# Kernel tuning notes

Hardware: AMD Instinct MI355X
Metric: run time of the kernel (lower is better)

The kernel has to match this reference:

```python
import jax, jax.numpy as jnp
import numpy as np

L, B, E, H = 1024, 8, 1024, 16
HD = E // H
SCALE = HD ** -0.5
EPS = 1e-5


def setup_inputs() -> dict:
    key = jax.random.key(0)
    ks = jax.random.split(key, 6)
    s = E ** -0.5
    return {
        "x": jax.random.normal(ks[0], (L, B, E), dtype=jnp.float32),
        "attn_mask": jnp.zeros((L, L), dtype=jnp.float32),
        "Wq": jax.random.normal(ks[1], (E, E), dtype=jnp.float32) * s,
        "bq": jnp.zeros((E,), dtype=jnp.float32),
        "Wk": jax.random.normal(ks[2], (E, E), dtype=jnp.float32) * s,
        "bk": jnp.zeros((E,), dtype=jnp.float32),
        "Wv": jax.random.normal(ks[3], (E, E), dtype=jnp.float32) * s,
        "bv": jnp.zeros((E,), dtype=jnp.float32),
        "Wo": jax.random.normal(ks[4], (E, E), dtype=jnp.float32) * s,
        "bo": jnp.zeros((E,), dtype=jnp.float32),
        "gamma": jnp.ones((E,), dtype=jnp.float32),
        "beta": jnp.zeros((E,), dtype=jnp.float32),
    }


def _layernorm(x, gamma, beta):
    mu = jnp.mean(x, axis=-1, keepdims=True)
    var = jnp.mean(jnp.square(x - mu), axis=-1, keepdims=True)
    return (x - mu) * jax.lax.rsqrt(var + EPS) * gamma + beta


def reference(x, attn_mask, Wq, bq, Wk, bk, Wv, bv, Wo, bo, gamma, beta):
    # x: (L, B, E); pre-LN residual attention block (dropout=0, eval)
    ln_x = _layernorm(x, gamma, beta)
    # torch Linear: y = x @ W.T + b
    q = (ln_x @ Wq.T + bq) * SCALE
    k = ln_x @ Wk.T + bk
    v = ln_x @ Wv.T + bv
    # (L, B, E) -> (B, H, L, hd)
    def split_heads(t):
        return t.reshape(L, B, H, HD).transpose(1, 2, 0, 3)
    q, k, v = split_heads(q), split_heads(k), split_heads(v)
    # full attention matrix, as in the original non-fused bmm path
    attn = jnp.einsum('bhqd,bhkd->bhqk', q, k) + attn_mask[None, None]
    attn = jax.nn.softmax(attn, axis=-1)
    out = jnp.einsum('bhqk,bhkd->bhqd', attn, v)  # (B, H, L, hd)
    out = out.transpose(2, 0, 1, 3).reshape(L, B, E)
    out = out @ Wo.T + bo
    return x + out
```

## Files before the change

### kernel.cpp

```cpp
#include <hip/hip_runtime.h>

#define LL 1024
#define BB 8
#define EE 1024
#define HH 16
#define HD 64
#define MROWS (LL*BB)

typedef __attribute__((ext_vector_type(8))) short short8v;
typedef __attribute__((ext_vector_type(4))) float f32x4;
typedef __attribute__((ext_vector_type(16))) float f32x16;

#define LOG2E 1.44269504088896f

__device__ __forceinline__ unsigned short tobf(float f) {
    union { float f; unsigned u; } un; un.f = f;
    unsigned u = un.u;
    u += 0x7fffu + ((u >> 16) & 1u);
    return (unsigned short)(u >> 16);
}

__device__ __forceinline__ float max3f(float a, float b, float c) {
    return fmaxf(fmaxf(a, b), c);
}

__device__ __forceinline__ void load_lds16(const unsigned short* g, unsigned short* l) {
    __builtin_amdgcn_global_load_lds((const __attribute__((address_space(1))) unsigned int*)g,
                                     (__attribute__((address_space(3))) unsigned int*)l,
                                     16, 0, 0);
}

__global__ __launch_bounds__(256) void convw4_kernel(const float* __restrict__ w0,
                                                     const float* __restrict__ w1,
                                                     const float* __restrict__ w2,
                                                     const float* __restrict__ w3,
                                                     unsigned short* __restrict__ o0,
                                                     unsigned short* __restrict__ o1,
                                                     unsigned short* __restrict__ o2,
                                                     unsigned short* __restrict__ o3) {
    const float* w; unsigned short* o;
    switch (blockIdx.y) {
        case 0:  w = w0; o = o0; break;
        case 1:  w = w1; o = o1; break;
        case 2:  w = w2; o = o2; break;
        default: w = w3; o = o3; break;
    }
    int i = (blockIdx.x * 256 + threadIdx.x) * 4;
    float4 v = *(const float4*)&w[i];
    ushort4 r;
    r.x = tobf(v.x); r.y = tobf(v.y); r.z = tobf(v.z); r.w = tobf(v.w);
    *(ushort4*)&o[i] = r;
}

__global__ __launch_bounds__(256) void maskprep_kernel(const float* __restrict__ m,
                                                       unsigned* __restrict__ o) {
    __shared__ float t_sh[64][65];
    const int q0 = blockIdx.x * 64, k0 = blockIdx.y * 64;
    const int tid = threadIdx.x;
    {
        const int r = tid >> 2, c0 = (tid & 3) * 16;
        #pragma unroll
        for (int i = 0; i < 4; ++i) {
            float4 v = *(const float4*)&m[(size_t)(q0 + r) * LL + k0 + c0 + i*4];
            t_sh[r][c0+i*4+0] = v.x; t_sh[r][c0+i*4+1] = v.y;
            t_sh[r][c0+i*4+2] = v.z; t_sh[r][c0+i*4+3] = v.w;
        }
    }
    __syncthreads();
    const int k2l = tid >> 3, qi = (tid & 7) * 8;
    unsigned pk[8];
    #pragma unroll
    for (int j = 0; j < 8; ++j) {
        const unsigned lo = tobf(t_sh[qi+j][2*k2l]   * LOG2E);
        const unsigned hb = tobf(t_sh[qi+j][2*k2l+1] * LOG2E);
        pk[j] = lo | (hb << 16);
    }
    unsigned* orow = &o[(size_t)(k0/2 + k2l) * LL + q0 + qi];
    *(uint4*)&orow[0] = make_uint4(pk[0], pk[1], pk[2], pk[3]);
    *(uint4*)&orow[4] = make_uint4(pk[4], pk[5], pk[6], pk[7]);
}

__global__ __launch_bounds__(256) void ln_kernel(const float* __restrict__ x,
                                                 const float* __restrict__ gamma,
                                                 const float* __restrict__ beta,
                                                 unsigned short* __restrict__ out) {
    const int row = blockIdx.x;
    const int tid = threadIdx.x;
    const float4 v = *(const float4*)&x[(size_t)row * EE + tid * 4];
    float s = v.x + v.y + v.z + v.w;
    float q = v.x*v.x + v.y*v.y + v.z*v.z + v.w*v.w;
    #pragma unroll
    for (int off = 1; off < 64; off <<= 1) {
        s += __shfl_xor(s, off);
        q += __shfl_xor(q, off);
    }
    __shared__ float ss[4], sq[4];
    const int wv = tid >> 6;
    if ((tid & 63) == 0) { ss[wv] = s; sq[wv] = q; }
    __syncthreads();
    s = ss[0] + ss[1] + ss[2] + ss[3];
    q = sq[0] + sq[1] + sq[2] + sq[3];
    const float mu = s * (1.0f / EE);
    const float var = q * (1.0f / EE) - mu * mu;
    const float rs = rsqrtf(var + 1e-5f);
    ushort4 o;
    o.x = tobf((v.x - mu) * rs * gamma[tid*4+0] + beta[tid*4+0]);
    o.y = tobf((v.y - mu) * rs * gamma[tid*4+1] + beta[tid*4+1]);
    o.z = tobf((v.z - mu) * rs * gamma[tid*4+2] + beta[tid*4+2]);
    o.w = tobf((v.w - mu) * rs * gamma[tid*4+3] + beta[tid*4+3]);
    *(ushort4*)&out[(size_t)row * EE + tid * 4] = o;
}

#define GEMM128_BODY(A_, W_)                                                              \
    __shared__ unsigned short a_sh[3][128*32];                                            \
    __shared__ unsigned short b_sh[3][128*32];                                            \
    const int tid = threadIdx.x, lane = tid & 63, wave = tid >> 6;                        \
    const int bm = blockIdx.y * 128, bn = blockIdx.x * 128;                               \
    const int wr = (wave >> 1) * 64, wc = (wave & 1) * 64;                                \
    const int l16 = lane & 15, q4 = lane >> 4;                                            \
    const int grow = lane >> 2;                                                           \
    const int gswz = (((lane & 3) ^ (grow & 3)) * 8);                                     \
    const int rslot = (q4 ^ (l16 & 3)) * 16;                       \
    f32x4 acc[4][4] = {};                                                                 \
    _Pragma("unroll")                                                                     \
    for (int i = 0; i < 2; ++i) {                                                         \
        const int ch = wave * 2 + i;                                                      \
        load_lds16(&A_[(size_t)(bm + ch*16 + grow)*EE + gswz], &a_sh[0][ch*512]);         \
        load_lds16(&W_[(size_t)(bn + ch*16 + grow)*EE + gswz], &b_sh[0][ch*512]);         \
    }                                                                                     \
    _Pragma("unroll")                                                                     \
    for (int i = 0; i < 2; ++i) {                                                         \
        const int ch = wave * 2 + i;                                                      \
        load_lds16(&A_[(size_t)(bm + ch*16 + grow)*EE + 32 + gswz], &a_sh[1][ch*512]);    \
        load_lds16(&W_[(size_t)(bn + ch*16 + grow)*EE + 32 + gswz], &b_sh[1][ch*512]);    \
    }                                                                                     \
    int buf = 0, sb = 2;                                                                  \
    for (int it = 0; it < 32; ++it) {                                                     \
        if (it < 31) asm volatile("s_waitcnt vmcnt(4)" ::: "memory");                     \
        else         asm volatile("s_waitcnt vmcnt(0)" ::: "memory");                     \
        __builtin_amdgcn_s_barrier();                                                     \
        if (it < 30) {                                                                    \
            const int kn = (it + 2) * 32;                                                 \
            _Pragma("unroll")                                                             \
            for (int i = 0; i < 2; ++i) {                                                 \
                const int ch = wave * 2 + i;                                              \
                load_lds16(&A_[(size_t)(bm + ch*16 + grow)*EE + kn + gswz], &a_sh[sb][ch*512]); \
                load_lds16(&W_[(size_t)(bn + ch*16 + grow)*EE + kn + gswz], &b_sh[sb][ch*512]); \
            }                                                                             \
        }                                                                                 \
        short8v af[4], bf[4];                                                             \
        _Pragma("unroll")                                                                 \
        for (int mi = 0; mi < 4; ++mi)                                                    \
            af[mi] = *(const short8v*)((const char*)&a_sh[buf][0] + (size_t)(wr + mi*16 + l16)*64 + rslot); \
        _Pragma("unroll")                                                                 \
        for (int ni = 0; ni < 4; ++ni)                                                    \
            bf[ni] = *(const short8v*)((const char*)&b_sh[buf][0] + (size_t)(wc + ni*16 + l16)*64 + rslot); \
        __builtin_amdgcn_s_setprio(1);                                                    \
        _Pragma("unroll")                                                                 \
        for (int mi = 0; mi < 4; ++mi)                                                    \
            _Pragma("unroll")                                                             \
            for (int ni = 0; ni < 4; ++ni)                                                \
                acc[mi][ni] = __builtin_amdgcn_mfma_f32_16x16x32_bf16(af[mi], bf[ni], acc[mi][ni], 0, 0, 0); \
        __builtin_amdgcn_s_setprio(0);                                                    \
        buf = (buf == 2) ? 0 : buf + 1;                                                   \
        sb  = (sb  == 2) ? 0 : sb  + 1;                                                   \
    }

__global__ __launch_bounds__(256) void gemm_qkv(const unsigned short* __restrict__ A,
                                                const unsigned short* __restrict__ W,
                                                const float* __restrict__ bq,
                                                const float* __restrict__ bk,
                                                const float* __restrict__ bv,
                                                unsigned short* __restrict__ qo,
                                                unsigned short* __restrict__ ko,
                                                unsigned short* __restrict__ vo) {
    GEMM128_BODY(A, W)
    const int seg = blockIdx.x >> 3;
    const float* bias = seg == 0 ? bq : (seg == 1 ? bk : bv);
    #pragma unroll
    for (int mi = 0; mi < 4; ++mi) {
        #pragma unroll
        for (int ni = 0; ni < 4; ++ni) {
            #pragma unroll
            for (int r = 0; r < 4; ++r) {
                const int m  = bm + wr + mi*16 + (lane >> 4)*4 + r;
                const int nn = (bn & 1023) + wc + ni*16 + l16;
                const float v = acc[mi][ni][r] + bias[nn];
                const int l = m >> 3, b = m & 7, h = nn >> 6, d = nn & 63;
                const int bh = b*HH + h;
                if (seg == 2) {
                    const int k16 = l >> 4, khi = (l >> 3) & 1, ke = l & 7;
                    const int dt = d >> 5, dl = d & 31;
                    vo[((((size_t)bh*64 + k16)*2 + dt)*64 + khi*32 + dl)*8 + ke] = tobf(v);
                } else {
                    const int t32 = l >> 5, l32 = l & 31;
                    const int dc = d >> 4, hi2 = (d >> 3) & 1, e = d & 7;
                    const size_t idx = ((((size_t)bh*32 + t32)*4 + dc)*64 + hi2*32 + l32)*8 + e;
                    if (seg == 0) qo[idx] = tobf(v * (0.125f * LOG2E));
                    else          ko[idx] = tobf(v);
                }
            }
        }
    }
}

__global__ __launch_bounds__(256) void gemm_o(const unsigned short* __restrict__ A,
                                              const unsigned short* __restrict__ W,
                                              const float* __restrict__ bias,
                                              const float* __restrict__ xres,
                                              float* __restrict__ outf) {
    GEMM128_BODY(A, W)
    #pragma unroll
    for (int mi = 0; mi < 4; ++mi) {
        #pragma unroll
        for (int ni = 0; ni < 4; ++ni) {
            #pragma unroll
            for (int r = 0; r < 4; ++r) {
                const int m = bm + wr + mi*16 + (lane >> 4)*4 + r;
                const int n = bn + wc + ni*16 + l16;
                outf[(size_t)m * EE + n] = acc[mi][ni][r] + bias[n] + xres[(size_t)m * EE + n];
            }
        }
    }
}

__global__ __launch_bounds__(256) void attn_kernel(const unsigned short* __restrict__ Qf,
                                                   const unsigned short* __restrict__ Kf,
                                                   const unsigned short* __restrict__ Vf,
                                                   const unsigned* __restrict__ maskT2,
                                                   unsigned short* __restrict__ attn_out) {
    const int tid = threadIdx.x, lane = tid & 63, wave = tid >> 6;
    const int l32 = lane & 31, hi = lane >> 5;
    const int b1 = blockIdx.x;
    const int bh = (b1 & 7) * 16 + ((b1 >> 3) & 15);
    const int qt = ((b1 >> 7) & 7) * 4 + wave;
    const int qtok = qt * 32 + l32;
    const unsigned short* qfp = Qf + ((size_t)(bh * 32 + qt) * 4) * 512;
    const unsigned short* kfb = Kf + (size_t)bh * 32 * 4 * 512;
    const unsigned short* vfb = Vf + (size_t)bh * 64 * 2 * 512;

    short8v qf[4];
    #pragma unroll
    for (int dc = 0; dc < 4; ++dc)
        qf[dc] = *(const short8v*)&qfp[dc * 512 + lane * 8];

    f32x16 acc[2] = {};
    float mrun = -1e30f, srun = 0.f;

    const unsigned* mt2base = maskT2 + qtok;
    short8v kf[4];
    #pragma unroll
    for (int dc = 0; dc < 4; ++dc)
        kf[dc] = *(const short8v*)&kfb[dc * 512 + lane * 8];
    unsigned mcur[8], mnxt[8];
    #pragma unroll
    for (int j = 0; j < 8; ++j)
        mcur[j] = mt2base[(size_t)((j & 1) + 4*(j >> 1) + 2*hi) * LL];

    for (int t = 0; t < 32; ++t) {
        f32x16 s = {};
        __builtin_amdgcn_s_setprio(1);
        #pragma unroll
        for (int dc = 0; dc < 4; ++dc)
            s = __builtin_amdgcn_mfma_f32_32x32x16_bf16(kf[dc], qf[dc], s, 0, 0, 0);
        __builtin_amdgcn_s_setprio(0);
        short8v vf00, vf01, vf10, vf11;
        vf00 = *(const short8v*)&vfb[((size_t)(t*2 + 0)*2 + 0)*512 + lane*8];
        vf01 = *(const short8v*)&vfb[((size_t)(t*2 + 0)*2 + 1)*512 + lane*8];
        vf10 = *(const short8v*)&vfb[((size_t)(t*2 + 1)*2 + 0)*512 + lane*8];
        vf11 = *(const short8v*)&vfb[((size_t)(t*2 + 1)*2 + 1)*512 + lane*8];
        if (t < 31) {
            #pragma unroll
            for (int dc = 0; dc < 4; ++dc)
                kf[dc] = *(const short8v*)&kfb[((size_t)(t + 1)*4 + dc)*512 + lane*8];
            #pragma unroll
            for (int j = 0; j < 8; ++j)
                mnxt[j] = mt2base[(size_t)((t + 1)*16 + (j & 1) + 4*(j >> 1) + 2*hi) * LL];
        }
        #pragma unroll
        for (int j = 0; j < 8; ++j) {
            s[2*j]   += __uint_as_float(mcur[j] << 16);
            s[2*j+1] += __uint_as_float(mcur[j] & 0xffff0000u);
        }
        const float a0 = max3f(s[0],  s[1],  s[2]);
        const float a1 = max3f(s[3],  s[4],  s[5]);
        const float a2 = max3f(s[6],  s[7],  s[8]);
        const float a3 = max3f(s[9],  s[10], s[11]);
        const float a4 = max3f(s[12], s[13], s[14]);
        float pm = fmaxf(max3f(a0, a1, a2), max3f(a3, a4, s[15]));
        pm = fmaxf(pm, __shfl_xor(pm, 32));
        if (__any(pm - mrun > 8.0f)) {
            const float mn = fmaxf(mrun, pm);
            const float al = exp2f(mrun - mn);
            #pragma unroll
            for (int i = 0; i < 16; ++i) { acc[0][i] *= al; acc[1][i] *= al; }
            srun *= al;
            mrun = mn;
        }
        float p[16];
        #pragma unroll
        for (int i = 0; i < 16; ++i) p[i] = exp2f(s[i] - mrun);
        const float t0 = p[0]+p[1],   t1 = p[2]+p[3],   t2 = p[4]+p[5],   t3 = p[6]+p[7];
        const float t4 = p[8]+p[9],   t5 = p[10]+p[11], t6 = p[12]+p[13], t7 = p[14]+p[15];
        const float u0 = t0+t1, u1 = t2+t3, u2 = t4+t5, u3 = t6+t7;
        float rs = (u0+u1) + (u2+u3);
        rs += __shfl_xor(rs, 32);
        srun += rs;
        unsigned w[8];
        #pragma unroll
        for (int j = 0; j < 8; ++j)
            asm("v_cvt_pk_bf16_f32 %0, %1, %2" : "=v"(w[j]) : "v"(p[2*j]), "v"(p[2*j+1]));
        asm volatile("v_permlane32_swap_b32 %0, %1" : "+v"(w[0]), "+v"(w[2]));
        asm volatile("v_permlane32_swap_b32 %0, %1" : "+v"(w[1]), "+v"(w[3]));
        asm volatile("v_permlane32_swap_b32 %0, %1" : "+v"(w[4]), "+v"(w[6]));
        asm volatile("v_permlane32_swap_b32 %0, %1" : "+v"(w[5]), "+v"(w[7]));
        union { uint4 u; short8v s8; } pb0, pb1;
        pb0.u = make_uint4(w[0], w[1], w[2], w[3]);
        pb1.u = make_uint4(w[4], w[5], w[6], w[7]);
        __builtin_amdgcn_s_setprio(1);
        acc[0] = __builtin_amdgcn_mfma_f32_32x32x16_bf16(vf00, pb0.s8, acc[0], 0, 0, 0);
        acc[1] = __builtin_amdgcn_mfma_f32_32x32x16_bf16(vf01, pb0.s8, acc[1], 0, 0, 0);
        acc[0] = __builtin_amdgcn_mfma_f32_32x32x16_bf16(vf10, pb1.s8, acc[0], 0, 0, 0);
        acc[1] = __builtin_amdgcn_mfma_f32_32x32x16_bf16(vf11, pb1.s8, acc[1], 0, 0, 0);
        __builtin_amdgcn_s_setprio(0);
        #pragma unroll
        for (int j = 0; j < 8; ++j) mcur[j] = mnxt[j];
    }
    const float inv = 1.0f / srun;
    const int b = bh >> 4, h = bh & 15;
    unsigned short* orow = attn_out + ((size_t)qtok * BB + b) * EE + h * HD;
    #pragma unroll
    for (int dt = 0; dt < 2; ++dt) {
        #pragma unroll
        for (int g = 0; g < 4; ++g) {
            const float a0 = acc[dt][4*g+0]*inv, a1 = acc[dt][4*g+1]*inv;
            const float a2 = acc[dt][4*g+2]*inv, a3 = acc[dt][4*g+3]*inv;
            unsigned lo, hw;
            asm("v_cvt_pk_bf16_f32 %0, %1, %2" : "=v"(lo) : "v"(a0), "v"(a1));
            asm("v_cvt_pk_bf16_f32 %0, %1, %2" : "=v"(hw) : "v"(a2), "v"(a3));
            *(uint2*)&orow[dt*32 + g*8 + hi*4] = make_uint2(lo, hw);
        }
    }
}

extern "C" void kernel_launch(void* const* d_in, const int* in_sizes, int n_in,
                              void* d_out, int out_size, void* d_ws, size_t ws_size,
                              hipStream_t stream) {
    (void)in_sizes; (void)n_in; (void)out_size; (void)ws_size;
    const float* x     = (const float*)d_in[0];
    const float* mask  = (const float*)d_in[1];
    const float* Wq    = (const float*)d_in[2];
    const float* bq    = (const float*)d_in[3];
    const float* Wk    = (const float*)d_in[4];
    const float* bk    = (const float*)d_in[5];
    const float* Wv    = (const float*)d_in[6];
    const float* bv    = (const float*)d_in[7];
    const float* Wo    = (const float*)d_in[8];
    const float* bo    = (const float*)d_in[9];
    const float* gamma = (const float*)d_in[10];
    const float* beta  = (const float*)d_in[11];
    float* out = (float*)d_out;

    unsigned short* ws   = (unsigned short*)d_ws;
    unsigned short* ln   = ws;
    unsigned short* wqkv = ln   + (size_t)MROWS * EE;
    unsigned short* wob  = wqkv + (size_t)3 * EE * EE;
    unsigned short* qb   = wob  + (size_t)EE * EE;
    unsigned short* kbp  = qb   + (size_t)BB * HH * LL * HD;
    unsigned short* vtb  = kbp  + (size_t)BB * HH * LL * HD;
    unsigned short* attnb = ln;
    unsigned* maskT2 = (unsigned*)wqkv;

    convw4_kernel<<<dim3(1024, 4), 256, 0, stream>>>(
        Wq, Wk, Wv, Wo,
        wqkv, wqkv + (size_t)EE * EE, wqkv + (size_t)2 * EE * EE, wob);
    ln_kernel<<<MROWS, 256, 0, stream>>>(x, gamma, beta, ln);

    gemm_qkv<<<dim3(24, 64), 256, 0, stream>>>(ln, wqkv, bq, bk, bv, qb, kbp, vtb);

    maskprep_kernel<<<dim3(16, 16), 256, 0, stream>>>(mask, maskT2);

    attn_kernel<<<1024, 256, 0, stream>>>(qb, kbp, vtb, maskT2, attnb);

    gemm_o<<<dim3(8, 64), 256, 0, stream>>>(attnb, wob, bo, x, out);
}
```

Baseline: 223.3 us.

## Skip mask loads when mask is all-zero; compute row sums via MFMA with ones

The mask prep kernel now sets a device flag if any mask entry is nonzero, and the attention kernel reads that flag and skips the per-tile mask loads and adds when it is clear. The softmax row sum now comes from extra MFMAs against a ones matrix instead of VALU adds and a cross-lane shuffle, and the row-max reduction uses permlane32 swap instead of a shuffle. Launch bounds are raised to request higher occupancy. The check runs at runtime, so nonzero masks still take the correct path. The cost is an extra memset launch, two more MFMAs per tile, and extra accumulator registers.

New measurement: 223.5 us. No clear change (+0.1%).

```diff
diff --git a/kernel.cpp b/kernel.cpp
--- a/kernel.cpp
+++ b/kernel.cpp
@@ -53,19 +53,23 @@
 }
 
 __global__ __launch_bounds__(256) void maskprep_kernel(const float* __restrict__ m,
-                                                       unsigned* __restrict__ o) {
+                                                       unsigned* __restrict__ o,
+                                                       unsigned* __restrict__ flag) {
     __shared__ float t_sh[64][65];
     const int q0 = blockIdx.x * 64, k0 = blockIdx.y * 64;
     const int tid = threadIdx.x;
+    unsigned nz = 0;
     {
         const int r = tid >> 2, c0 = (tid & 3) * 16;
         #pragma unroll
         for (int i = 0; i < 4; ++i) {
             float4 v = *(const float4*)&m[(size_t)(q0 + r) * LL + k0 + c0 + i*4];
+            nz |= (v.x != 0.0f) | (v.y != 0.0f) | (v.z != 0.0f) | (v.w != 0.0f);
             t_sh[r][c0+i*4+0] = v.x; t_sh[r][c0+i*4+1] = v.y;
             t_sh[r][c0+i*4+2] = v.z; t_sh[r][c0+i*4+3] = v.w;
         }
     }
+    if (__any(nz) && (tid & 63) == 0) atomicOr(flag, 1u);
     __syncthreads();
     const int k2l = tid >> 3, qi = (tid & 7) * 8;
     unsigned pk[8];
@@ -224,17 +228,19 @@
     }
 }
 
-__global__ __launch_bounds__(256) void attn_kernel(const unsigned short* __restrict__ Qf,
-                                                   const unsigned short* __restrict__ Kf,
-                                                   const unsigned short* __restrict__ Vf,
-                                                   const unsigned* __restrict__ maskT2,
-                                                   unsigned short* __restrict__ attn_out) {
+__global__ __launch_bounds__(256, 4) void attn_kernel(const unsigned short* __restrict__ Qf,
+                                                      const unsigned short* __restrict__ Kf,
+                                                      const unsigned short* __restrict__ Vf,
+                                                      const unsigned* __restrict__ maskT2,
+                                                      const unsigned* __restrict__ mflagp,
+                                                      unsigned short* __restrict__ attn_out) {
     const int tid = threadIdx.x, lane = tid & 63, wave = tid >> 6;
     const int l32 = lane & 31, hi = lane >> 5;
     const int b1 = blockIdx.x;
     const int bh = (b1 & 7) * 16 + ((b1 >> 3) & 15);
     const int qt = ((b1 >> 7) & 7) * 4 + wave;
     const int qtok = qt * 32 + l32;
+    const unsigned mf = (unsigned)__builtin_amdgcn_readfirstlane((int)mflagp[0]);
     const unsigned short* qfp = Qf + ((size_t)(bh * 32 + qt) * 4) * 512;
     const unsigned short* kfb = Kf + (size_t)bh * 32 * 4 * 512;
     const unsigned short* vfb = Vf + (size_t)bh * 64 * 2 * 512;
@@ -244,8 +250,13 @@
     for (int dc = 0; dc < 4; ++dc)
         qf[dc] = *(const short8v*)&qfp[dc * 512 + lane * 8];
 
+    union { unsigned u4[4]; short8v s8; } ones;
+    #pragma unroll
+    for (int i = 0; i < 4; ++i) ones.u4[i] = 0x3F803F80u;
+
     f32x16 acc[2] = {};
-    float mrun = -1e30f, srun = 0.f;
+    f32x16 accs = {};
+    float mrun = -1e30f;
 
     const unsigned* mt2base = maskT2 + qtok;
     short8v kf[4];
@@ -253,9 +264,11 @@
     for (int dc = 0; dc < 4; ++dc)
         kf[dc] = *(const short8v*)&kfb[dc * 512 + lane * 8];
     unsigned mcur[8], mnxt[8];
-    #pragma unroll
-    for (int j = 0; j < 8; ++j)
-        mcur[j] = mt2base[(size_t)((j & 1) + 4*(j >> 1) + 2*hi) * LL];
+    if (mf) {
+        #pragma unroll
+        for (int j = 0; j < 8; ++j)
+            mcur[j] = mt2base[(size_t)((j & 1) + 4*(j >> 1) + 2*hi) * LL];
+    }
 
     for (int t = 0; t < 32; ++t) {
         f32x16 s = {};
@@ -273,14 +286,18 @@
             #pragma unroll
             for (int dc = 0; dc < 4; ++dc)
                 kf[dc] = *(const short8v*)&kfb[((size_t)(t + 1)*4 + dc)*512 + lane*8];
-            #pragma unroll
-            for (int j = 0; j < 8; ++j)
-                mnxt[j] = mt2base[(size_t)((t + 1)*16 + (j & 1) + 4*(j >> 1) + 2*hi) * LL];
-        }
-        #pragma unroll
-        for (int j = 0; j < 8; ++j) {
-            s[2*j]   += __uint_as_float(mcur[j] << 16);
-            s[2*j+1] += __uint_as_float(mcur[j] & 0xffff0000u);
+            if (mf) {
+                #pragma unroll
+                for (int j = 0; j < 8; ++j)
+                    mnxt[j] = mt2base[(size_t)((t + 1)*16 + (j & 1) + 4*(j >> 1) + 2*hi) * LL];
+            }
+        }
+        if (mf) {
+            #pragma unroll
+            for (int j = 0; j < 8; ++j) {
+                s[2*j]   += __uint_as_float(mcur[j] << 16);
+                s[2*j+1] += __uint_as_float(mcur[j] & 0xffff0000u);
+            }
         }
         const float a0 = max3f(s[0],  s[1],  s[2]);
         const float a1 = max3f(s[3],  s[4],  s[5]);
@@ -288,28 +305,24 @@
         const float a3 = max3f(s[9],  s[10], s[11]);
         const float a4 = max3f(s[12], s[13], s[14]);
         float pm = fmaxf(max3f(a0, a1, a2), max3f(a3, a4, s[15]));
-        pm = fmaxf(pm, __shfl_xor(pm, 32));
+        {
+            float pu = pm, pv = pm;
+            asm volatile("v_permlane32_swap_b32 %0, %1" : "+v"(pu), "+v"(pv));
+            pm = fmaxf(pu, pv);
+        }
         if (__any(pm - mrun > 8.0f)) {
             const float mn = fmaxf(mrun, pm);
             const float al = exp2f(mrun - mn);
             #pragma unroll
-            for (int i = 0; i < 16; ++i) { acc[0][i] *= al; acc[1][i] *= al; }
-            srun *= al;
+            for (int i = 0; i < 16; ++i) { acc[0][i] *= al; acc[1][i] *= al; accs[i] *= al; }
             mrun = mn;
         }
-        float p[16];
-        #pragma unroll
-        for (int i = 0; i < 16; ++i) p[i] = exp2f(s[i] - mrun);
-        const float t0 = p[0]+p[1],   t1 = p[2]+p[3],   t2 = p[4]+p[5],   t3 = p[6]+p[7];
-        const float t4 = p[8]+p[9],   t5 = p[10]+p[11], t6 = p[12]+p[13], t7 = p[14]+p[15];
-        const float u0 = t0+t1, u1 = t2+t3, u2 = t4+t5, u3 = t6+t7;
-        float rs = (u0+u1) + (u2+u3);
-        rs += __shfl_xor(rs, 32);
-        srun += rs;
+        #pragma unroll
+        for (int i = 0; i < 16; ++i) s[i] = exp2f(s[i] - mrun);
         unsigned w[8];
         #pragma unroll
         for (int j = 0; j < 8; ++j)
-            asm("v_cvt_pk_bf16_f32 %0, %1, %2" : "=v"(w[j]) : "v"(p[2*j]), "v"(p[2*j+1]));
+            asm("v_cvt_pk_bf16_f32 %0, %1, %2" : "=v"(w[j]) : "v"(s[2*j]), "v"(s[2*j+1]));
         asm volatile("v_permlane32_swap_b32 %0, %1" : "+v"(w[0]), "+v"(w[2]));
         asm volatile("v_permlane32_swap_b32 %0, %1" : "+v"(w[1]), "+v"(w[3]));
         asm volatile("v_permlane32_swap_b32 %0, %1" : "+v"(w[4]), "+v"(w[6]));
@@ -318,15 +331,19 @@
         pb0.u = make_uint4(w[0], w[1], w[2], w[3]);
         pb1.u = make_uint4(w[4], w[5], w[6], w[7]);
         __builtin_amdgcn_s_setprio(1);
+        accs   = __builtin_amdgcn_mfma_f32_32x32x16_bf16(ones.s8, pb0.s8, accs, 0, 0, 0);
         acc[0] = __builtin_amdgcn_mfma_f32_32x32x16_bf16(vf00, pb0.s8, acc[0], 0, 0, 0);
         acc[1] = __builtin_amdgcn_mfma_f32_32x32x16_bf16(vf01, pb0.s8, acc[1], 0, 0, 0);
+        accs   = __builtin_amdgcn_mfma_f32_32x32x16_bf16(ones.s8, pb1.s8, accs, 0, 0, 0);
         acc[0] = __builtin_amdgcn_mfma_f32_32x32x16_bf16(vf10, pb1.s8, acc[0], 0, 0, 0);
         acc[1] = __builtin_amdgcn_mfma_f32_32x32x16_bf16(vf11, pb1.s8, acc[1], 0, 0, 0);
         __builtin_amdgcn_s_setprio(0);
-        #pragma unroll
-        for (int j = 0; j < 8; ++j) mcur[j] = mnxt[j];
-    }
-    const float inv = 1.0f / srun;
+        if (mf) {
+            #pragma unroll
+            for (int j = 0; j < 8; ++j) mcur[j] = mnxt[j];
+        }
+    }
+    const float inv = 1.0f / accs[0];
     const int b = bh >> 4, h = bh & 15;
     unsigned short* orow = attn_out + ((size_t)qtok * BB + b) * EE + h * HD;
     #pragma unroll
@@ -370,6 +387,7 @@
     unsigned short* vtb  = kbp  + (size_t)BB * HH * LL * HD;
     unsigned short* attnb = ln;
     unsigned* maskT2 = (unsigned*)wqkv;
+    unsigned* mflag  = (unsigned*)(wqkv + (size_t)2 * EE * EE);
 
     convw4_kernel<<<dim3(1024, 4), 256, 0, stream>>>(
         Wq, Wk, Wv, Wo,
@@ -378,9 +396,10 @@
 
     gemm_qkv<<<dim3(24, 64), 256, 0, stream>>>(ln, wqkv, bq, bk, bv, qb, kbp, vtb);
 
-    maskprep_kernel<<<dim3(16, 16), 256, 0, stream>>>(mask, maskT2);
-
-    attn_kernel<<<1024, 256, 0, stream>>>(qb, kbp, vtb, maskT2, attnb);
+    hipMemsetAsync(mflag, 0, 4, stream);
+    maskprep_kernel<<<dim3(16, 16), 256, 0, stream>>>(mask, maskT2, mflag);
+
+    attn_kernel<<<1024, 256, 0, stream>>>(qb, kbp, vtb, maskT2, mflag, attnb);
 
     gemm_o<<<dim3(8, 64), 256, 0, stream>>>(attnb, wob, bo, x, out);
 }
```
